# Optimization experiments

Hardware: AMD Instinct MI355X
Metric: run time of the kernel (lower is better)

The kernel has to match this reference:

```python
import jax, jax.numpy as jnp
import numpy as np
from jax import lax

PATCH = 32  # enc conv kernel/stride
EPS = 1e-12  # F.normalize eps


def setup_inputs() -> dict:
    key = jax.random.key(0)
    ks = jax.random.split(key, 7)
    B, N, H, W = 32, 256, 32, 32
    fdim, vdim = 512, 128
    x = jax.random.normal(ks[0], (B, 3 * N, H, W), dtype=jnp.float32)
    conv_w = jax.random.normal(ks[1], (fdim, 3, PATCH, PATCH), dtype=jnp.float32) * (1.0 / np.sqrt(3 * PATCH * PATCH))
    conv_b = jax.random.normal(ks[2], (fdim,), dtype=jnp.float32) * 0.01
    fc1_w = jax.random.normal(ks[3], (vdim, fdim), dtype=jnp.float32) * (1.0 / np.sqrt(fdim))
    fc1_b = jax.random.normal(ks[4], (vdim,), dtype=jnp.float32) * 0.01
    # deterministic dropout masks (p=0.5, train mode -> keep * 1/(1-p))
    drop1 = (jax.random.uniform(ks[5], (B, N, N)) >= 0.5).astype(jnp.float32) * 2.0
    drop2 = (jax.random.uniform(ks[6], (B, N, N)) >= 0.5).astype(jnp.float32) * 2.0
    return {"x": x, "conv_w": conv_w, "conv_b": conv_b,
            "fc1_w": fc1_w, "fc1_b": fc1_b, "drop1": drop1, "drop2": drop2}


def _branch(scores, drop, eye):
    # softmax over dim=-2, zero diag, dropout, L1-normalize over dim=-2
    P = jax.nn.softmax(scores, axis=-2)
    P = P * (1.0 - eye)
    P = P * drop
    denom = jnp.maximum(jnp.sum(jnp.abs(P), axis=-2, keepdims=True), EPS)
    return P / denom


def reference(x, conv_w, conv_b, fc1_w, fc1_b, drop1, drop2):
    B, C, H, W = x.shape
    N = C // 3
    xi = x.reshape(B * N, 3, H, W)
    # enc: patchify conv -> (B*N, fdim, 1, 1)
    fm = lax.conv_general_dilated(xi, conv_w, (PATCH, PATCH), 'VALID',
                                  dimension_numbers=('NCHW', 'OIHW', 'NCHW'))
    fm = fm + conv_b[None, :, None, None]
    # map2vec: adaptive avgpool(1,1) + flatten + fc1
    v = fm.mean(axis=(2, 3))                      # (B*N, fdim)
    v = v @ fc1_w.T + fc1_b                       # (B*N, vdim)
    f = v.reshape(B, N, -1)                       # (B, N, vdim)
    f_norm = f / jnp.maximum(jnp.linalg.norm(f, axis=-1, keepdims=True), EPS)
    A = jnp.einsum('bnd,bmd->bnm', f_norm, f_norm)  # cosine affinity (B,N,N)
    Atemp = A * (128.0 ** 0.5)                    # torch.div(A, 1/128**0.5)
    eye = jnp.eye(N, dtype=A.dtype)
    A1 = _branch(Atemp, drop1, eye)
    A2t = _branch(jnp.swapaxes(Atemp, -1, -2), drop2, eye)
    AtA = jnp.swapaxes(jnp.matmul(A2t, A1), -1, -2)
    # nll_loss(AtA, arange targets) == -mean of diagonal entries
    diag = jnp.einsum('bii->bi', AtA)
    loss = -jnp.mean(diag)
    return f, A, loss
```

## Files before the change

### kernel.cpp

```cpp
#include <hip/hip_runtime.h>
#include <stdint.h>

#define S_SCALE 11.313708498984761f
#define EPS 1e-12f

typedef __bf16 bf16x8 __attribute__((ext_vector_type(8)));
typedef float  f32x4  __attribute__((ext_vector_type(4)));

__device__ __forceinline__ f32x4 mfma16(bf16x8 a, bf16x8 b, f32x4 c) {
  return __builtin_amdgcn_mfma_f32_16x16x32_bf16(a, b, c, 0, 0, 0);
}

__device__ __forceinline__ float waveSum(float v) {
#pragma unroll
  for (int m = 32; m > 0; m >>= 1) v += __shfl_xor(v, m, 64);
  return v;
}

__device__ __forceinline__ void load_lds16(const float* g, float* l) {
  __builtin_amdgcn_global_load_lds(
      (const __attribute__((address_space(1))) uint32_t*)g,
      (__attribute__((address_space(3))) uint32_t*)l, 16, 0, 0);
}

#define OFF_W    0
#define OFF_BIAS 786432
#define OFF_FN   786944
#define OFF_ZP   2884096

__global__ __launch_bounds__(256) void k_prep(const float* __restrict__ conv_w,
                                              const float* __restrict__ fc1_w,
                                              const float* __restrict__ conv_b,
                                              const float* __restrict__ fc1_b,
                                              __bf16* __restrict__ W,
                                              float* __restrict__ bias2,
                                              float* __restrict__ loss) {
  __shared__ float cw_s[64][36];
  __shared__ float fc1_s[64][65];
  __shared__ float red[4];
  const int t = threadIdx.x;
  if (blockIdx.x >= 192) {
    const int o = blockIdx.x - 192;
    if (o == 0 && t == 0) loss[0] = 0.f;
    float p = fc1_w[o * 512 + t] * conv_b[t] +
              fc1_w[o * 512 + 256 + t] * conv_b[256 + t];
    p = waveSum(p);
    if ((t & 63) == 0) red[t >> 6] = p;
    __syncthreads();
    if (t == 0) bias2[o] = red[0] + red[1] + red[2] + red[3] + fc1_b[o];
    return;
  }
  const int oh = blockIdx.x & 1;
  const int kt = blockIdx.x >> 1;
  const int k0 = kt * 32, o0 = oh * 64;
  const int og = t >> 3, kg = t & 7;
  float acc[2][4] = {};
  for (int cs = 0; cs < 8; ++cs) {
    const int cc = cs * 64;
    __syncthreads();
#pragma unroll
    for (int i = 0; i < 8; ++i) {
      int idx = t + 256 * i;
      int cr = idx >> 5, kk = idx & 31;
      cw_s[cr][kk] = conv_w[(cc + cr) * 3072 + k0 + kk];
    }
#pragma unroll
    for (int i = 0; i < 4; ++i) {
      int idx = t + 256 * i;
      int o = idx >> 4, c4 = (idx & 15) * 4;
      float4 v = *(const float4*)&fc1_w[(o0 + o) * 512 + cc + c4];
      fc1_s[o][c4 + 0] = v.x; fc1_s[o][c4 + 1] = v.y;
      fc1_s[o][c4 + 2] = v.z; fc1_s[o][c4 + 3] = v.w;
    }
    __syncthreads();
    for (int ci = 0; ci < 64; ++ci) {
      float4 cw = *(const float4*)&cw_s[ci][kg * 4];
#pragma unroll
      for (int j = 0; j < 2; ++j) {
        float fv = fc1_s[og * 2 + j][ci];
        acc[j][0] = fmaf(fv, cw.x, acc[j][0]);
        acc[j][1] = fmaf(fv, cw.y, acc[j][1]);
        acc[j][2] = fmaf(fv, cw.z, acc[j][2]);
        acc[j][3] = fmaf(fv, cw.w, acc[j][3]);
      }
    }
  }
#pragma unroll
  for (int j = 0; j < 2; ++j)
#pragma unroll
    for (int q = 0; q < 4; ++q)
      W[(o0 + og * 2 + j) * 3072 + k0 + kg * 4 + q] = (__bf16)acc[j][q];
}

__device__ __forceinline__ void loadB(const __bf16* __restrict__ bp, int k0,
                                      uint4 (&dst)[2][2]) {
#pragma unroll
  for (int ks = 0; ks < 2; ++ks)
#pragma unroll
    for (int ni = 0; ni < 2; ++ni)
      dst[ks][ni] = *(const uint4*)(bp + ni * 16 * 3072 + k0 + ks * 32);
}

__device__ __forceinline__ void computeTile16(const float* __restrict__ Abuf,
                                              const uint4 (&breg)[2][2],
                                              int l15, int quad,
                                              f32x4 (&acc)[2]) {
  const int rb = l15 * 64;
#pragma unroll
  for (int ks = 0; ks < 2; ++ks) {
    float4 lo = *(const float4*)&Abuf[rb + (((ks * 8 + quad * 2 + 0) ^ l15) << 2)];
    float4 hi = *(const float4*)&Abuf[rb + (((ks * 8 + quad * 2 + 1) ^ l15) << 2)];
    union { __bf16 h[8]; bf16x8 v; } pk;
    pk.h[0] = (__bf16)lo.x; pk.h[1] = (__bf16)lo.y;
    pk.h[2] = (__bf16)lo.z; pk.h[3] = (__bf16)lo.w;
    pk.h[4] = (__bf16)hi.x; pk.h[5] = (__bf16)hi.y;
    pk.h[6] = (__bf16)hi.z; pk.h[7] = (__bf16)hi.w;
    bf16x8 af = pk.v;
#pragma unroll
    for (int ni = 0; ni < 2; ++ni)
      acc[ni] = mfma16(af, *(const bf16x8*)&breg[ks][ni], acc[ni]);
  }
}

__global__ __launch_bounds__(256) void k_gemm1f(const float* __restrict__ x,
                                                const __bf16* __restrict__ W,
                                                const float* __restrict__ bias2,
                                                float* __restrict__ f,
                                                __bf16* __restrict__ fn) {
  __shared__ __align__(16) float A_lds[4][1024];
  __shared__ float rsum[16][5];
  __shared__ float rinv[16];
  const int t = threadIdx.x;
  const int wave = t >> 6, lane = t & 63;
  const int l15 = lane & 15, quad = lane >> 4;
  const int m0 = blockIdx.x * 16;
  const int dr = wave * 4 + (lane >> 4);
  const int dc = ((lane & 15) ^ (dr & 15)) * 4;
  const float* xrow = x + (m0 + dr) * 3072 + dc;
  const __bf16* bp = W + (wave * 32 + l15) * 3072 + quad * 8;

  f32x4 acc[2] = {{0.f, 0.f, 0.f, 0.f}, {0.f, 0.f, 0.f, 0.f}};
  uint4 brA[2][2], brB[2][2];

  loadB(bp, 0, brA);
  load_lds16(xrow + 0 * 64, &A_lds[0][wave * 256]);
  load_lds16(xrow + 1 * 64, &A_lds[1][wave * 256]);
  load_lds16(xrow + 2 * 64, &A_lds[2][wave * 256]);

  for (int it2 = 0; it2 < 24; ++it2) {
    const int T0 = it2 * 2, T1 = T0 + 1;
    asm volatile("s_waitcnt vmcnt(1)" ::: "memory");
    __builtin_amdgcn_s_barrier();
    __builtin_amdgcn_sched_barrier(0);
    loadB(bp, (T0 + 1) * 64, brB);
    __builtin_amdgcn_sched_barrier(0);
    {
      int dk = T0 + 3 > 47 ? 47 : T0 + 3;
      load_lds16(xrow + dk * 64, &A_lds[(T0 + 3) & 3][wave * 256]);
    }
    __builtin_amdgcn_sched_barrier(0);
    computeTile16(&A_lds[T0 & 3][0], brA, l15, quad, acc);
    asm volatile("s_waitcnt vmcnt(1)" ::: "memory");
    __builtin_amdgcn_s_barrier();
    __builtin_amdgcn_sched_barrier(0);
    {
      int bk = T1 + 1 > 47 ? 47 : T1 + 1;
      loadB(bp, bk * 64, brA);
    }
    __builtin_amdgcn_sched_barrier(0);
    {
      int dk = T1 + 3 > 47 ? 47 : T1 + 3;
      load_lds16(xrow + dk * 64, &A_lds[(T1 + 3) & 3][wave * 256]);
    }
    __builtin_amdgcn_sched_barrier(0);
    computeTile16(&A_lds[T1 & 3][0], brB, l15, quad, acc);
  }

  __syncthreads();
  const float b0 = bias2[wave * 32 + l15];
  const float b1 = bias2[wave * 32 + 16 + l15];
#pragma unroll
  for (int r = 0; r < 4; ++r) {
    acc[0][r] += b0;
    acc[1][r] += b1;
    float s = acc[0][r] * acc[0][r] + acc[1][r] * acc[1][r];
    s += __shfl_xor(s, 1, 64);
    s += __shfl_xor(s, 2, 64);
    s += __shfl_xor(s, 4, 64);
    s += __shfl_xor(s, 8, 64);
    if (l15 == 0) rsum[quad * 4 + r][wave] = s;
  }
  __syncthreads();
  if (t < 16) {
    float s = rsum[t][0] + rsum[t][1] + rsum[t][2] + rsum[t][3];
    rinv[t] = 1.f / fmaxf(sqrtf(s), EPS);
  }
  __syncthreads();
#pragma unroll
  for (int r = 0; r < 4; ++r) {
    const int row = quad * 4 + r;
    const float iv = rinv[row];
    const int g = (m0 + row) * 128 + wave * 32 + l15;
    f[g] = acc[0][r];
    fn[g] = (__bf16)(acc[0][r] * iv);
    f[g + 16] = acc[1][r];
    fn[g + 16] = (__bf16)(acc[1][r] * iv);
  }
}

__global__ __launch_bounds__(256) void k_gemm2(const __bf16* __restrict__ fn,
                                               const float* __restrict__ d1,
                                               const float* __restrict__ d2,
                                               float* __restrict__ Aout,
                                               float* __restrict__ Zp) {
  __shared__ __align__(16) __bf16 Li[64][136];
  __shared__ __align__(16) __bf16 Lj[64][136];
  __shared__ float zred[2][4][64];
  const int t = threadIdx.x;
  const int b = blockIdx.y;
  const int ti = blockIdx.x >> 2, tj = blockIdx.x & 3;
  const int i0 = ti * 64, j0 = tj * 64;
  const int wave = t >> 6, lane = t & 63;
  const int l15 = lane & 15, quad = lane >> 4;
  const __bf16* fb = fn + b * 32768;
#pragma unroll
  for (int i = 0; i < 4; ++i) {
    int idx = t + 256 * i;
    int r = idx >> 4, c8 = (idx & 15) * 8;
    *(uint4*)&Li[r][c8] = *(const uint4*)&fb[(i0 + r) * 128 + c8];
    *(uint4*)&Lj[r][c8] = *(const uint4*)&fb[(j0 + r) * 128 + c8];
  }
  __syncthreads();
  f32x4 acc[4] = {{0.f, 0.f, 0.f, 0.f}, {0.f, 0.f, 0.f, 0.f},
                  {0.f, 0.f, 0.f, 0.f}, {0.f, 0.f, 0.f, 0.f}};
#pragma unroll
  for (int ks = 0; ks < 4; ++ks) {
    bf16x8 af = *(const bf16x8*)&Li[wave * 16 + l15][ks * 32 + quad * 8];
#pragma unroll
    for (int nt = 0; nt < 4; ++nt) {
      bf16x8 bf = *(const bf16x8*)&Lj[nt * 16 + l15][ks * 32 + quad * 8];
      acc[nt] = mfma16(af, bf, acc[nt]);
    }
  }
  const int base = b * 65536;
  float* Ab = Aout + base;
  float z1c[4] = {0.f, 0.f, 0.f, 0.f}, z2c[4] = {0.f, 0.f, 0.f, 0.f};
#pragma unroll
  for (int nt = 0; nt < 4; ++nt) {
    int gj = j0 + nt * 16 + l15;
#pragma unroll
    for (int r = 0; r < 4; ++r) {
      int gi = i0 + wave * 16 + quad * 4 + r;
      float a = acc[nt][r];
      Ab[gi * 256 + gj] = a;
      float e = __expf(fmaf(S_SCALE, a, -S_SCALE));
      if (gi != gj) {
        int idx = base + gi * 256 + gj;
        z1c[nt] = fmaf(e, d1[idx], z1c[nt]);
        z2c[nt] = fmaf(e, d2[idx], z2c[nt]);
      }
    }
  }
#pragma unroll
  for (int nt = 0; nt < 4; ++nt) {
    z1c[nt] += __shfl_xor(z1c[nt], 16, 64);
    z1c[nt] += __shfl_xor(z1c[nt], 32, 64);
    z2c[nt] += __shfl_xor(z2c[nt], 16, 64);
    z2c[nt] += __shfl_xor(z2c[nt], 32, 64);
  }
  if (quad == 0) {
#pragma unroll
    for (int nt = 0; nt < 4; ++nt) {
      zred[0][wave][nt * 16 + l15] = z1c[nt];
      zred[1][wave][nt * 16 + l15] = z2c[nt];
    }
  }
  __syncthreads();
  if (t < 128) {
    int z = t >> 6, c = t & 63;
    float s = zred[z][0][c] + zred[z][1][c] + zred[z][2][c] + zred[z][3][c];
    Zp[(z * 4 + ti) * 8192 + b * 256 + j0 + c] = s;
  }
}

__global__ __launch_bounds__(256) void k_loss(const float* __restrict__ Aout,
                                              const float* __restrict__ d1,
                                              const float* __restrict__ d2,
                                              const float* __restrict__ Zp,
                                              float* __restrict__ loss) {
  __shared__ float d1s[64][65];
  __shared__ float z1s[64], z2s[64];
  __shared__ float red[4];
  const int t = threadIdx.x;
  const int b = blockIdx.y;
  const int ic = blockIdx.x >> 2, kc = blockIdx.x & 3;
  const int i0 = ic * 64, k0 = kc * 64;
  const int base = b * 65536;
  if (t < 64) {
    float s = 0.f;
#pragma unroll
    for (int p = 0; p < 4; ++p) s += Zp[p * 8192 + b * 256 + i0 + t];
    z1s[t] = 1.f / fmaxf(s, EPS);
  } else if (t < 128) {
    float s = 0.f;
#pragma unroll
    for (int p = 0; p < 4; ++p) s += Zp[(4 + p) * 8192 + b * 256 + k0 + t - 64];
    z2s[t - 64] = 1.f / fmaxf(s, EPS);
  }
#pragma unroll
  for (int ii = 0; ii < 16; ++ii) {
    int idx = t + 256 * ii;
    int kr = idx >> 6, ci = idx & 63;
    d1s[kr][ci] = d1[base + (k0 + kr) * 256 + i0 + ci];
  }
  __syncthreads();
  const int kl = t & 63, ig = t >> 6;
  float inv2 = z2s[kl];
  float accv = 0.f;
  for (int ii = 0; ii < 16; ++ii) {
    int il = ig * 16 + ii;
    int idx = base + (i0 + il) * 256 + k0 + kl;
    float a = Aout[idx];
    float e = __expf(fmaf(2.f * S_SCALE, a, -2.f * S_SCALE));
    float v = e * d2[idx] * d1s[kl][il] * z1s[il] * inv2;
    if (i0 + il != k0 + kl) accv += v;
  }
  accv = waveSum(accv);
  if ((t & 63) == 0) red[t >> 6] = accv;
  __syncthreads();
  if (t == 0) {
    float tot = red[0] + red[1] + red[2] + red[3];
    atomicAdd(loss, tot * (-1.f / 8192.f));
  }
}

extern "C" void kernel_launch(void* const* d_in, const int* in_sizes, int n_in,
                              void* d_out, int out_size, void* d_ws,
                              size_t ws_size, hipStream_t stream) {
  const float* x = (const float*)d_in[0];
  const float* conv_w = (const float*)d_in[1];
  const float* conv_b = (const float*)d_in[2];
  const float* fc1_w = (const float*)d_in[3];
  const float* fc1_b = (const float*)d_in[4];
  const float* drop1 = (const float*)d_in[5];
  const float* drop2 = (const float*)d_in[6];
  char* ws = (char*)d_ws;
  __bf16* W = (__bf16*)(ws + OFF_W);
  float* bias2 = (float*)(ws + OFF_BIAS);
  __bf16* fn = (__bf16*)(ws + OFF_FN);
  float* Zp = (float*)(ws + OFF_ZP);
  float* f = (float*)d_out;
  float* Aout = f + 1048576;
  float* loss = f + 3145728;

  k_prep<<<320, 256, 0, stream>>>(conv_w, fc1_w, conv_b, fc1_b, W, bias2, loss);
  k_gemm1f<<<512, 256, 0, stream>>>(x, W, bias2, f, fn);
  k_gemm2<<<dim3(16, 32), 256, 0, stream>>>(fn, drop1, drop2, Aout, Zp);
  k_loss<<<dim3(16, 32), 256, 0, stream>>>(Aout, drop1, drop2, Zp, loss);
}
```

Baseline: 248.2 us.

## Restructure gemm1 main loop into 4-tile burst double-buffered pipeline

Replaces the fine-grained per-tile pipeline (a 4-deep LDS ring with vmcnt waits and a barrier every 64-K tile) with bursts of four K-tiles. Each burst is double-buffered in LDS and registers, so there are two __syncthreads per 512 K instead of eight barriers. LDS use doubles to 32KB and B-register staging quadruples; launch_bounds(256,2) is added to cap registers at two blocks per CU. The goal is fewer barriers and more outstanding loads, at the cost of register pressure and occupancy.

```diff
diff --git a/kernel.cpp b/kernel.cpp
--- a/kernel.cpp
+++ b/kernel.cpp
@@ -92,15 +92,6 @@
       W[(o0 + og * 2 + j) * 3072 + k0 + kg * 4 + q] = (__bf16)acc[j][q];
 }
 
-__device__ __forceinline__ void loadB(const __bf16* __restrict__ bp, int k0,
-                                      uint4 (&dst)[2][2]) {
-#pragma unroll
-  for (int ks = 0; ks < 2; ++ks)
-#pragma unroll
-    for (int ni = 0; ni < 2; ++ni)
-      dst[ks][ni] = *(const uint4*)(bp + ni * 16 * 3072 + k0 + ks * 32);
-}
-
 __device__ __forceinline__ void computeTile16(const float* __restrict__ Abuf,
                                               const uint4 (&breg)[2][2],
                                               int l15, int quad,
@@ -122,12 +113,12 @@
   }
 }
 
-__global__ __launch_bounds__(256) void k_gemm1f(const float* __restrict__ x,
-                                                const __bf16* __restrict__ W,
-                                                const float* __restrict__ bias2,
-                                                float* __restrict__ f,
-                                                __bf16* __restrict__ fn) {
-  __shared__ __align__(16) float A_lds[4][1024];
+__global__ __launch_bounds__(256, 2) void k_gemm1f(const float* __restrict__ x,
+                                                   const __bf16* __restrict__ W,
+                                                   const float* __restrict__ bias2,
+                                                   float* __restrict__ f,
+                                                   __bf16* __restrict__ fn) {
+  __shared__ __align__(16) float A_lds[2][4][1024];
   __shared__ float rsum[16][5];
   __shared__ float rinv[16];
   const int t = threadIdx.x;
@@ -140,43 +131,49 @@
   const __bf16* bp = W + (wave * 32 + l15) * 3072 + quad * 8;
 
   f32x4 acc[2] = {{0.f, 0.f, 0.f, 0.f}, {0.f, 0.f, 0.f, 0.f}};
-  uint4 brA[2][2], brB[2][2];
-
-  loadB(bp, 0, brA);
-  load_lds16(xrow + 0 * 64, &A_lds[0][wave * 256]);
-  load_lds16(xrow + 1 * 64, &A_lds[1][wave * 256]);
-  load_lds16(xrow + 2 * 64, &A_lds[2][wave * 256]);
-
-  for (int it2 = 0; it2 < 24; ++it2) {
-    const int T0 = it2 * 2, T1 = T0 + 1;
-    asm volatile("s_waitcnt vmcnt(1)" ::: "memory");
-    __builtin_amdgcn_s_barrier();
+  uint4 bX[4][2][2], bY[4][2][2];
+
+  auto burstD = [&](int S, int half) {
+#pragma unroll
+    for (int i = 0; i < 4; ++i)
+      load_lds16(xrow + S * 256 + i * 64, &A_lds[half][i][wave * 256]);
+  };
+  auto loadB4 = [&](int S, uint4(&d)[4][2][2]) {
+#pragma unroll
+    for (int i = 0; i < 4; ++i)
+#pragma unroll
+      for (int ks = 0; ks < 2; ++ks)
+#pragma unroll
+        for (int ni = 0; ni < 2; ++ni)
+          d[i][ks][ni] =
+              *(const uint4*)(bp + ni * 16 * 3072 + S * 256 + i * 64 + ks * 32);
+  };
+  auto compute4 = [&](int half, const uint4(&d)[4][2][2]) {
+#pragma unroll
+    for (int i = 0; i < 4; ++i)
+      computeTile16(&A_lds[half][i][0], d[i], l15, quad, acc);
+  };
+
+  burstD(0, 0);
+  loadB4(0, bX);
+  __syncthreads();
+
+  for (int s2 = 0; s2 < 6; ++s2) {
+    const int S0 = s2 * 2;
+    burstD(S0 + 1, 1);
+    loadB4(S0 + 1, bY);
     __builtin_amdgcn_sched_barrier(0);
-    loadB(bp, (T0 + 1) * 64, brB);
+    compute4(0, bX);
+    __syncthreads();
+    if (s2 < 5) {
+      burstD(S0 + 2, 0);
+      loadB4(S0 + 2, bX);
+    }
     __builtin_amdgcn_sched_barrier(0);
-    {
-      int dk = T0 + 3 > 47 ? 47 : T0 + 3;
-      load_lds16(xrow + dk * 64, &A_lds[(T0 + 3) & 3][wave * 256]);
-    }
-    __builtin_amdgcn_sched_barrier(0);
-    computeTile16(&A_lds[T0 & 3][0], brA, l15, quad, acc);
-    asm volatile("s_waitcnt vmcnt(1)" ::: "memory");
-    __builtin_amdgcn_s_barrier();
-    __builtin_amdgcn_sched_barrier(0);
-    {
-      int bk = T1 + 1 > 47 ? 47 : T1 + 1;
-      loadB(bp, bk * 64, brA);
-    }
-    __builtin_amdgcn_sched_barrier(0);
-    {
-      int dk = T1 + 3 > 47 ? 47 : T1 + 3;
-      load_lds16(xrow + dk * 64, &A_lds[(T1 + 3) & 3][wave * 256]);
-    }
-    __builtin_amdgcn_sched_barrier(0);
-    computeTile16(&A_lds[T1 & 3][0], brB, l15, quad, acc);
-  }
-
-  __syncthreads();
+    compute4(1, bY);
+    __syncthreads();
+  }
+
   const float b0 = bias2[wave * 32 + l15];
   const float b1 = bias2[wave * 32 + 16 + l15];
 #pragma unroll
```

After: 244.8 us. About the same (-1.4%).
